# Performance work log

Measured on AMD Instinct MI355X. Metric: run time of the kernel, lower is better.

Reference implementation:

```python
import jax, jax.numpy as jnp
import numpy as np

N_NODES = 50000
N_EDGES = 800000
N_FIELDS = 4
N_MESH = 8
HIDDEN = 128
IN_CH = N_FIELDS * 1 + N_MESH  # 12


def _w(key, shape, scale=0.05):
    return jax.random.normal(key, shape, dtype=jnp.float32) * scale


def setup_inputs() -> dict:
    key = jax.random.key(0)
    ks = jax.random.split(key, 20)
    inp = {
        "F_0": jax.random.normal(ks[0], (N_NODES, 1, N_FIELDS), dtype=jnp.float32),
        "meshfield": jax.random.normal(ks[1], (N_NODES, N_MESH), dtype=jnp.float32),
        "edge_index": jax.random.randint(ks[2], (2, N_EDGES), 0, N_NODES, dtype=jnp.int32),
        "n_timesteps": 8,
        # encoder SAGEConv 1: in 12 -> 128 ; SAGEConv 2: 128 -> 128
        "enc1_Wl": _w(ks[3], (HIDDEN, IN_CH)), "enc1_bl": jnp.zeros((HIDDEN,), jnp.float32), "enc1_Wr": _w(ks[4], (HIDDEN, IN_CH)),
        "enc2_Wl": _w(ks[5], (HIDDEN, HIDDEN)), "enc2_bl": jnp.zeros((HIDDEN,), jnp.float32), "enc2_Wr": _w(ks[6], (HIDDEN, HIDDEN)),
        # decoder SAGEConv 1 & 2: 128 -> 128
        "dec1_Wl": _w(ks[7], (HIDDEN, HIDDEN)), "dec1_bl": jnp.zeros((HIDDEN,), jnp.float32), "dec1_Wr": _w(ks[8], (HIDDEN, HIDDEN)),
        "dec2_Wl": _w(ks[9], (HIDDEN, HIDDEN)), "dec2_bl": jnp.zeros((HIDDEN,), jnp.float32), "dec2_Wr": _w(ks[10], (HIDDEN, HIDDEN)),
        # output head: 128 -> n_fields
        "lin_W": _w(ks[11], (N_FIELDS, HIDDEN)), "lin_b": jnp.zeros((N_FIELDS,), jnp.float32),
    }
    return inp


def sage_conv(x, src, dst, Wl, bl, Wr, n_nodes):
    # PyG SAGEConv: out = lin_l(mean_j x_j) + lin_r(x_i); lin_l has bias, lin_r does not.
    msg = x[src]                                             # [E, C] gather
    agg = jax.ops.segment_sum(msg, dst, num_segments=n_nodes)
    cnt = jax.ops.segment_sum(jnp.ones((src.shape[0], 1), x.dtype), dst, num_segments=n_nodes)
    agg = agg / jnp.maximum(cnt, 1.0)                        # scatter-mean
    return agg @ Wl.T + bl + x @ Wr.T


def reference(F_0, meshfield, edge_index, n_timesteps,
              enc1_Wl, enc1_bl, enc1_Wr, enc2_Wl, enc2_bl, enc2_Wr,
              dec1_Wl, dec1_bl, dec1_Wr, dec2_Wl, dec2_bl, dec2_Wr,
              lin_W, lin_b):
    n = F_0.shape[0]
    src, dst = edge_index[0], edge_index[1]
    relu = jax.nn.relu
    F_prev = F_0  # [N, n_prev=1, n_fields]
    outs = []
    for _ in range(int(n_timesteps)):
        x_prev = F_prev[:, -1]                               # [N, n_fields]
        x = jnp.concatenate([F_prev.reshape(n, -1), meshfield], axis=1)  # [N, 12]
        # encoder GraphSAGE (act between layers, none after last)
        h = relu(sage_conv(x, src, dst, enc1_Wl, enc1_bl, enc1_Wr, n))
        h = sage_conv(h, src, dst, enc2_Wl, enc2_bl, enc2_Wr, n)
        h = relu(h)                                          # self.act after encoder
        # decoder GraphSAGE
        h = relu(sage_conv(h, src, dst, dec1_Wl, dec1_bl, dec1_Wr, n))
        h = sage_conv(h, src, dst, dec2_Wl, dec2_bl, dec2_Wr, n)
        h = relu(h)                                          # self.act after decoder
        x_new = x_prev + h @ lin_W.T + lin_b                 # residual update
        outs.append(x_new[:, None, :])
        # recurrence uses detached prediction (x.detach() in torch)
        F_prev = jnp.concatenate([F_prev[:, 1:], jax.lax.stop_gradient(x_new)[:, None, :]], axis=1)
    return jnp.concatenate(outs, axis=1)                     # [N, n_timesteps, n_fields]
```

## Files before the change

kernel.cpp:

```cpp
#include <hip/hip_runtime.h>


typedef __attribute__((ext_vector_type(8))) short short8;
typedef __attribute__((ext_vector_type(8))) unsigned short ushort8;
typedef __attribute__((ext_vector_type(4))) float f32x4;

static __device__ __forceinline__ float b2f(unsigned short u) {
  return __uint_as_float(((unsigned int)u) << 16);
}
static __device__ __forceinline__ unsigned short f2bf(float f) {
  unsigned int u = __float_as_uint(f);
  u += 0x7FFFu + ((u >> 16) & 1u);
  return (unsigned short)(u >> 16);
}


__global__ void count_rank_kernel(const int* __restrict__ dst, int* __restrict__ cnt,
                                  int* __restrict__ rank, int E) {
  int e = blockIdx.x * blockDim.x + threadIdx.x;
  if (e < E) rank[e] = atomicAdd(&cnt[dst[e]], 1);
}

__global__ __launch_bounds__(256) void blocksum_kernel(const int* __restrict__ cnt,
                                                       int* __restrict__ bsum, int n) {
  __shared__ int s[256];
  int tid = threadIdx.x;
  int i = blockIdx.x * 256 + tid;
  s[tid] = (i < n) ? cnt[i] : 0;
  __syncthreads();
  for (int off = 128; off > 0; off >>= 1) {
    if (tid < off) s[tid] += s[tid + off];
    __syncthreads();
  }
  if (tid == 0) bsum[blockIdx.x] = s[0];
}

__global__ __launch_bounds__(256) void scan_sums_kernel(const int* __restrict__ bsum,
                                                        int* __restrict__ boff, int nb) {
  __shared__ int s[256];
  int tid = threadIdx.x;
  int v = (tid < nb) ? bsum[tid] : 0;
  s[tid] = v;
  __syncthreads();
  for (int off = 1; off < 256; off <<= 1) {
    int t = (tid >= off) ? s[tid - off] : 0;
    __syncthreads();
    s[tid] += t;
    __syncthreads();
  }
  if (tid < nb) boff[tid] = s[tid] - v;
}

__global__ __launch_bounds__(256) void expand_kernel(const int* __restrict__ cnt,
                                                     const int* __restrict__ boff,
                                                     int* __restrict__ row_ptr,
                                                     float* __restrict__ rdeg, int n) {
  __shared__ int s[256];
  int tid = threadIdx.x;
  int i = blockIdx.x * 256 + tid;
  int v = (i < n) ? cnt[i] : 0;
  s[tid] = v;
  __syncthreads();
  for (int off = 1; off < 256; off <<= 1) {
    int t = (tid >= off) ? s[tid - off] : 0;
    __syncthreads();
    s[tid] += t;
    __syncthreads();
  }
  if (i < n) {
    row_ptr[i + 1] = boff[blockIdx.x] + s[tid];
    rdeg[i] = 1.0f / fmaxf((float)v, 1.0f);
  }
  if (i == 0) row_ptr[0] = 0;
}

__global__ void fill_csr2_kernel(const int* __restrict__ src, const int* __restrict__ dst,
                                 const int* __restrict__ rank, const int* __restrict__ row_ptr,
                                 int* __restrict__ col, int E) {
  int e = blockIdx.x * blockDim.x + threadIdx.x;
  if (e < E) col[row_ptr[dst[e]] + rank[e]] = src[e];
}

__global__ void f2bf6_kernel(const float* __restrict__ s0, const float* __restrict__ s1,
                             const float* __restrict__ s2, const float* __restrict__ s3,
                             const float* __restrict__ s4, const float* __restrict__ s5,
                             unsigned short* __restrict__ dst) {
  int i = blockIdx.x * blockDim.x + threadIdx.x;
  if (i >= 6 * 16384) return;
  int m = i >> 14, o = i & 16383;
  const float* s;
  switch (m) {
    case 0: s = s0; break; case 1: s = s1; break; case 2: s = s2; break;
    case 3: s = s3; break; case 4: s = s4; break; default: s = s5; break;
  }
  dst[i] = f2bf(s[o]);
}

__global__ void aggmesh_kernel(const float* __restrict__ mesh, float* __restrict__ aggm,
                               const int* __restrict__ row_ptr, const int* __restrict__ col,
                               const float* __restrict__ rdeg, int N) {
  int g = blockIdx.x * blockDim.x + threadIdx.x;
  int node = g >> 1, h = (g & 1) * 4;
  if (node >= N) return;
  int j0 = row_ptr[node], j1 = row_ptr[node + 1];
  float4 acc = make_float4(0.f, 0.f, 0.f, 0.f);
  int j = j0;
  for (; j + 4 <= j1; j += 4) {
    float4 v0 = *(const float4*)&mesh[col[j] * 8 + h];
    float4 v1 = *(const float4*)&mesh[col[j + 1] * 8 + h];
    float4 v2 = *(const float4*)&mesh[col[j + 2] * 8 + h];
    float4 v3 = *(const float4*)&mesh[col[j + 3] * 8 + h];
    acc.x += (v0.x + v1.x) + (v2.x + v3.x);
    acc.y += (v0.y + v1.y) + (v2.y + v3.y);
    acc.z += (v0.z + v1.z) + (v2.z + v3.z);
    acc.w += (v0.w + v1.w) + (v2.w + v3.w);
  }
  for (; j < j1; ++j) {
    float4 v0 = *(const float4*)&mesh[col[j] * 8 + h];
    acc.x += v0.x; acc.y += v0.y; acc.z += v0.z; acc.w += v0.w;
  }
  float r = rdeg[node];
  acc.x *= r; acc.y *= r; acc.z *= r; acc.w *= r;
  *(float4*)&aggm[node * 8 + h] = acc;
}

__global__ void mesh_term_kernel(const float* __restrict__ aggm, const float* __restrict__ mesh,
                                 const float* __restrict__ Wl, const float* __restrict__ Wr,
                                 const float* __restrict__ bl, unsigned short* __restrict__ mterm,
                                 int N) {
  int g = blockIdx.x * blockDim.x + threadIdx.x;
  if (g >= N * 128) return;
  int n = g >> 7, o = g & 127;
  float acc = bl[o];
#pragma unroll
  for (int k = 0; k < 8; ++k)
    acc += Wl[o * 12 + 4 + k] * aggm[n * 8 + k] + Wr[o * 12 + 4 + k] * mesh[n * 8 + k];
  mterm[g] = f2bf(acc);
}


__global__ __launch_bounds__(256) void enc1_kernel(
    const float* __restrict__ xprev, const int* __restrict__ row_ptr,
    const int* __restrict__ col, const float* __restrict__ rdeg,
    const float* __restrict__ Wl, const float* __restrict__ Wr,
    const unsigned short* __restrict__ mterm, unsigned short* __restrict__ out, int N) {
  __shared__ float Wx[8][128];
  __shared__ float4 part[256];
  __shared__ float As[64][8];
  int tid = threadIdx.x;
  int nb = blockIdx.x * 64;
  for (int i = tid; i < 1024; i += 256) {
    int k = i >> 7, o = i & 127;
    Wx[k][o] = (k < 4) ? Wl[o * 12 + k] : Wr[o * 12 + (k - 4)];
  }
  int nl = tid >> 2, q = tid & 3;
  int gn = nb + nl; if (gn > N - 1) gn = N - 1;
  int j0 = row_ptr[gn], j1 = row_ptr[gn + 1];
  int per = (j1 - j0 + 3) >> 2;
  int a = j0 + q * per; if (a > j1) a = j1;
  int b = a + per; if (b > j1) b = j1;
  float4 acc = make_float4(0.f, 0.f, 0.f, 0.f);
  int j = a;
  for (; j + 2 <= b; j += 2) {
    float4 v0 = *(const float4*)&xprev[col[j] * 4];
    float4 v1 = *(const float4*)&xprev[col[j + 1] * 4];
    acc.x += v0.x + v1.x; acc.y += v0.y + v1.y;
    acc.z += v0.z + v1.z; acc.w += v0.w + v1.w;
  }
  if (j < b) {
    float4 v0 = *(const float4*)&xprev[col[j] * 4];
    acc.x += v0.x; acc.y += v0.y; acc.z += v0.z; acc.w += v0.w;
  }
  part[tid] = acc;
  __syncthreads();
  if (tid < 64) {
    int g2 = nb + tid; if (g2 > N - 1) g2 = N - 1;
    float4 s0 = part[tid * 4], s1 = part[tid * 4 + 1];
    float4 s2 = part[tid * 4 + 2], s3 = part[tid * 4 + 3];
    float r = rdeg[g2];
    As[tid][0] = (s0.x + s1.x + s2.x + s3.x) * r;
    As[tid][1] = (s0.y + s1.y + s2.y + s3.y) * r;
    As[tid][2] = (s0.z + s1.z + s2.z + s3.z) * r;
    As[tid][3] = (s0.w + s1.w + s2.w + s3.w) * r;
    float4 own = *(const float4*)&xprev[g2 * 4];
    As[tid][4] = own.x; As[tid][5] = own.y; As[tid][6] = own.z; As[tid][7] = own.w;
  }
  __syncthreads();
  int gn2 = nb + nl;
  if (gn2 >= N) return;
  float av[8];
#pragma unroll
  for (int k = 0; k < 8; ++k) av[k] = As[nl][k];
  int o0 = q * 32;
#pragma unroll
  for (int c = 0; c < 4; ++c) {
    ushort8 mt = *(const ushort8*)&mterm[gn2 * 128 + o0 + c * 8];
    ushort8 ov;
#pragma unroll
    for (int oo = 0; oo < 8; ++oo) {
      int o = o0 + c * 8 + oo;
      float s = b2f(mt[oo]);
#pragma unroll
      for (int k = 0; k < 8; ++k) s += av[k] * Wx[k][o];
      ov[oo] = f2bf(fmaxf(s, 0.0f));
    }
    *(ushort8*)&out[gn2 * 128 + o0 + c * 8] = ov;
  }
}

__global__ void agg128_kernel(const unsigned short* __restrict__ feat,
                              unsigned short* __restrict__ out,
                              const int* __restrict__ row_ptr, const int* __restrict__ col,
                              const float* __restrict__ rdeg, int N) {
  int g = blockIdx.x * blockDim.x + threadIdx.x;
  int node = g >> 4;
  int d = g & 15;
  if (node >= N) return;
  int j0 = row_ptr[node], j1 = row_ptr[node + 1];
  float acc[8] = {};
  int j = j0;
  for (; j + 8 <= j1; j += 8) {
    ushort8 v0 = *(const ushort8*)&feat[col[j    ] * 128 + d * 8];
    ushort8 v1 = *(const ushort8*)&feat[col[j + 1] * 128 + d * 8];
    ushort8 v2 = *(const ushort8*)&feat[col[j + 2] * 128 + d * 8];
    ushort8 v3 = *(const ushort8*)&feat[col[j + 3] * 128 + d * 8];
    ushort8 v4 = *(const ushort8*)&feat[col[j + 4] * 128 + d * 8];
    ushort8 v5 = *(const ushort8*)&feat[col[j + 5] * 128 + d * 8];
    ushort8 v6 = *(const ushort8*)&feat[col[j + 6] * 128 + d * 8];
    ushort8 v7 = *(const ushort8*)&feat[col[j + 7] * 128 + d * 8];
#pragma unroll
    for (int r = 0; r < 8; ++r)
      acc[r] += ((b2f(v0[r]) + b2f(v1[r])) + (b2f(v2[r]) + b2f(v3[r]))) +
                ((b2f(v4[r]) + b2f(v5[r])) + (b2f(v6[r]) + b2f(v7[r])));
  }
  for (; j + 2 <= j1; j += 2) {
    ushort8 v0 = *(const ushort8*)&feat[col[j] * 128 + d * 8];
    ushort8 v1 = *(const ushort8*)&feat[col[j + 1] * 128 + d * 8];
#pragma unroll
    for (int r = 0; r < 8; ++r) acc[r] += b2f(v0[r]) + b2f(v1[r]);
  }
  if (j < j1) {
    ushort8 v0 = *(const ushort8*)&feat[col[j] * 128 + d * 8];
#pragma unroll
    for (int r = 0; r < 8; ++r) acc[r] += b2f(v0[r]);
  }
  float rd = rdeg[node];
  ushort8 o;
#pragma unroll
  for (int r = 0; r < 8; ++r) o[r] = f2bf(acc[r] * rd);
  *(ushort8*)&out[node * 128 + d * 8] = o;
}

__global__ __launch_bounds__(256) void gemm128_mfma_kernel(
    const unsigned short* __restrict__ agg, const unsigned short* __restrict__ x,
    const unsigned short* __restrict__ Wlb, const unsigned short* __restrict__ Wrb,
    const float* __restrict__ bl, unsigned short* __restrict__ out, int N) {
  int tid = threadIdx.x;
  int wave = tid >> 6;
  int lane = tid & 63;
  int nb = blockIdx.x * 128 + wave * 32;
  int l15 = lane & 15;
  int lk = (lane >> 4) * 8;

  f32x4 acc[2][8] = {};
  int r0 = nb + l15;      if (r0 > N - 1) r0 = N - 1;
  int r1 = nb + 16 + l15; if (r1 > N - 1) r1 = N - 1;

#pragma unroll
  for (int ks = 0; ks < 8; ++ks) {
    const unsigned short* As = (ks < 4) ? agg : x;
    const unsigned short* Ws = (ks < 4) ? Wlb : Wrb;
    int ko = (ks & 3) * 32 + lk;
    short8 a0 = *(const short8*)&As[r0 * 128 + ko];
    short8 a1 = *(const short8*)&As[r1 * 128 + ko];
#pragma unroll
    for (int ot = 0; ot < 8; ++ot) {
      short8 b = *(const short8*)&Ws[(ot * 16 + l15) * 128 + ko];
      acc[0][ot] = __builtin_amdgcn_mfma_f32_16x16x32_bf16(a0, b, acc[0][ot], 0, 0, 0);
      acc[1][ot] = __builtin_amdgcn_mfma_f32_16x16x32_bf16(a1, b, acc[1][ot], 0, 0, 0);
    }
  }

  int crow = (lane >> 4) * 4;
#pragma unroll
  for (int ot = 0; ot < 8; ++ot) {
    int gcol = ot * 16 + l15;
    float bv = bl[gcol];
#pragma unroll
    for (int mt = 0; mt < 2; ++mt) {
#pragma unroll
      for (int r = 0; r < 4; ++r) {
        int grow = nb + mt * 16 + crow + r;
        if (grow < N) {
          float v = fmaxf(acc[mt][ot][r] + bv, 0.0f);
          out[grow * 128 + gcol] = f2bf(v);
        }
      }
    }
  }
}

__global__ __launch_bounds__(256) void gemm128_head_mfma_kernel(
    const unsigned short* __restrict__ agg, const unsigned short* __restrict__ x,
    const unsigned short* __restrict__ Wlb, const unsigned short* __restrict__ Wrb,
    const float* __restrict__ bl, const float* __restrict__ linW,
    const float* __restrict__ linb, float* __restrict__ xprev,
    float* __restrict__ out, int N, int T, int t) {
  __shared__ float Wh[4][128];
  int tid = threadIdx.x;
  for (int i = tid; i < 512; i += 256) Wh[i >> 7][i & 127] = linW[i];
  __syncthreads();

  int wave = tid >> 6;
  int lane = tid & 63;
  int nb = blockIdx.x * 128 + wave * 32;
  int l15 = lane & 15;
  int lk = (lane >> 4) * 8;

  f32x4 acc[2][8] = {};
  int r0 = nb + l15;      if (r0 > N - 1) r0 = N - 1;
  int r1 = nb + 16 + l15; if (r1 > N - 1) r1 = N - 1;

#pragma unroll
  for (int ks = 0; ks < 8; ++ks) {
    const unsigned short* As = (ks < 4) ? agg : x;
    const unsigned short* Ws = (ks < 4) ? Wlb : Wrb;
    int ko = (ks & 3) * 32 + lk;
    short8 a0 = *(const short8*)&As[r0 * 128 + ko];
    short8 a1 = *(const short8*)&As[r1 * 128 + ko];
#pragma unroll
    for (int ot = 0; ot < 8; ++ot) {
      short8 b = *(const short8*)&Ws[(ot * 16 + l15) * 128 + ko];
      acc[0][ot] = __builtin_amdgcn_mfma_f32_16x16x32_bf16(a0, b, acc[0][ot], 0, 0, 0);
      acc[1][ot] = __builtin_amdgcn_mfma_f32_16x16x32_bf16(a1, b, acc[1][ot], 0, 0, 0);
    }
  }

  float part[2][4][4] = {};
#pragma unroll
  for (int ot = 0; ot < 8; ++ot) {
    int gcol = ot * 16 + l15;
    float bv = bl[gcol];
    float w0 = Wh[0][gcol], w1 = Wh[1][gcol], w2 = Wh[2][gcol], w3 = Wh[3][gcol];
#pragma unroll
    for (int mt = 0; mt < 2; ++mt)
#pragma unroll
      for (int r = 0; r < 4; ++r) {
        float hv = fmaxf(acc[mt][ot][r] + bv, 0.0f);
        part[mt][r][0] += hv * w0;
        part[mt][r][1] += hv * w1;
        part[mt][r][2] += hv * w2;
        part[mt][r][3] += hv * w3;
      }
  }
#pragma unroll
  for (int m = 1; m < 16; m <<= 1)
#pragma unroll
    for (int mt = 0; mt < 2; ++mt)
#pragma unroll
      for (int r = 0; r < 4; ++r)
#pragma unroll
        for (int o = 0; o < 4; ++o)
          part[mt][r][o] += __shfl_xor(part[mt][r][o], m, 64);

  if (l15 == 0) {
    int crow = (lane >> 4) * 4;
    float4 lb = *(const float4*)linb;
#pragma unroll
    for (int mt = 0; mt < 2; ++mt)
#pragma unroll
      for (int r = 0; r < 4; ++r) {
        int grow = nb + mt * 16 + crow + r;
        if (grow < N) {
          float4 xp = *(const float4*)&xprev[grow * 4];
          float4 xn;
          xn.x = xp.x + part[mt][r][0] + lb.x;
          xn.y = xp.y + part[mt][r][1] + lb.y;
          xn.z = xp.z + part[mt][r][2] + lb.z;
          xn.w = xp.w + part[mt][r][3] + lb.w;
          *(float4*)&out[(grow * T + t) * 4] = xn;
          *(float4*)&xprev[grow * 4] = xn;
        }
      }
  }
}

extern "C" void kernel_launch(void* const* d_in, const int* in_sizes, int n_in,
                              void* d_out, int out_size, void* d_ws, size_t ws_size,
                              hipStream_t stream) {
  const float* F0   = (const float*)d_in[0];
  const float* mesh = (const float*)d_in[1];
  const int*   eidx = (const int*)d_in[2];
  const float* e1Wl = (const float*)d_in[4];
  const float* e1bl = (const float*)d_in[5];
  const float* e1Wr = (const float*)d_in[6];
  const float* e2Wl = (const float*)d_in[7];
  const float* e2bl = (const float*)d_in[8];
  const float* e2Wr = (const float*)d_in[9];
  const float* d1Wl = (const float*)d_in[10];
  const float* d1bl = (const float*)d_in[11];
  const float* d1Wr = (const float*)d_in[12];
  const float* d2Wl = (const float*)d_in[13];
  const float* d2bl = (const float*)d_in[14];
  const float* d2Wr = (const float*)d_in[15];
  const float* linW = (const float*)d_in[16];
  const float* linb = (const float*)d_in[17];

  const int N = in_sizes[0] / 4;
  const int E = in_sizes[2] / 2;
  const int T = out_size / (N * 4);
  const int* src = eidx;
  const int* dst = eidx + E;

  size_t off = 0;
  auto alloc = [&](size_t bytes) -> void* {
    void* p = (char*)d_ws + off;
    off += (bytes + 511) & ~(size_t)511;
    return p;
  };
  int*   cnt     = (int*)alloc((size_t)N * 4);
  int*   row_ptr = (int*)alloc((size_t)(N + 1) * 4);
  int*   rank    = (int*)alloc((size_t)E * 4);
  int*   col     = (int*)alloc((size_t)E * 4);
  float* rdeg    = (float*)alloc((size_t)N * 4);
  float* xprev   = (float*)alloc((size_t)N * 4 * 4);
  float* aggm    = (float*)alloc((size_t)N * 8 * 4);
  int*   bsum    = (int*)alloc(256 * 4);
  int*   boff    = (int*)alloc(256 * 4);
  unsigned short* mterm = (unsigned short*)alloc((size_t)N * 128 * 2);
  unsigned short* h1   = (unsigned short*)alloc((size_t)N * 128 * 2);
  unsigned short* h2   = (unsigned short*)alloc((size_t)N * 128 * 2);
  unsigned short* aggb = (unsigned short*)alloc((size_t)N * 128 * 2);
  unsigned short* wb   = (unsigned short*)alloc((size_t)6 * 128 * 128 * 2);
  unsigned short* e2Wlb = wb + 0 * 16384;
  unsigned short* e2Wrb = wb + 1 * 16384;
  unsigned short* d1Wlb = wb + 2 * 16384;
  unsigned short* d1Wrb = wb + 3 * 16384;
  unsigned short* d2Wlb = wb + 4 * 16384;
  unsigned short* d2Wrb = wb + 5 * 16384;

  float* outp = (float*)d_out;

  const int NB = (N + 255) / 256;

  hipMemsetAsync(cnt, 0, (size_t)N * 4, stream);
  count_rank_kernel<<<(E + 255) / 256, 256, 0, stream>>>(dst, cnt, rank, E);
  blocksum_kernel<<<NB, 256, 0, stream>>>(cnt, bsum, N);
  scan_sums_kernel<<<1, 256, 0, stream>>>(bsum, boff, NB);
  expand_kernel<<<NB, 256, 0, stream>>>(cnt, boff, row_ptr, rdeg, N);
  fill_csr2_kernel<<<(E + 255) / 256, 256, 0, stream>>>(src, dst, rank, row_ptr, col, E);
  f2bf6_kernel<<<(6 * 16384 + 255) / 256, 256, 0, stream>>>(
      e2Wl, e2Wr, d1Wl, d1Wr, d2Wl, d2Wr, wb);
  aggmesh_kernel<<<(N * 2 + 255) / 256, 256, 0, stream>>>(mesh, aggm, row_ptr, col, rdeg, N);
  mesh_term_kernel<<<(N * 128 + 255) / 256, 256, 0, stream>>>(aggm, mesh, e1Wl, e1Wr, e1bl,
                                                              mterm, N);
  hipMemcpyAsync(xprev, F0, (size_t)N * 4 * 4, hipMemcpyDeviceToDevice, stream);

  const int gAgg  = (N * 16 + 255) / 256;
  const int gGemm = (N + 127) / 128;
  const int gEnc1 = (N + 63) / 64;

  for (int t = 0; t < T; ++t) {
    enc1_kernel<<<gEnc1, 256, 0, stream>>>(xprev, row_ptr, col, rdeg,
                                           e1Wl, e1Wr, mterm, h1, N);

    agg128_kernel<<<gAgg, 256, 0, stream>>>(h1, aggb, row_ptr, col, rdeg, N);
    gemm128_mfma_kernel<<<gGemm, 256, 0, stream>>>(aggb, h1, e2Wlb, e2Wrb, e2bl, h2, N);

    agg128_kernel<<<gAgg, 256, 0, stream>>>(h2, aggb, row_ptr, col, rdeg, N);
    gemm128_mfma_kernel<<<gGemm, 256, 0, stream>>>(aggb, h2, d1Wlb, d1Wrb, d1bl, h1, N);

    agg128_kernel<<<gAgg, 256, 0, stream>>>(h1, aggb, row_ptr, col, rdeg, N);
    gemm128_head_mfma_kernel<<<gGemm, 256, 0, stream>>>(aggb, h1, d2Wlb, d2Wrb, d2bl,
                                                        linW, linb, xprev, outp, N, T, t);
  }
}
```

Measured before the change: 1.642 ms.

## Fuse neighbor mean aggregation into MFMA GEMM via LDS staging

Merges the separate 128-channel gather-mean kernel and the MFMA GEMM kernel into one kernel per SAGE layer. Each block aggregates 64 nodes into padded LDS and then runs the bf16 MFMA GEMM straight from LDS, so the aggregated intermediate no longer makes a round trip through global memory and the kernel launch count drops. The trade-off is smaller GEMM tiles (16 rows per wave instead of 32), which reloads the weights more often, and the gather and GEMM phases now share a block's occupancy, which could reduce latency hiding during the irregular gathers.

```diff
diff --git a/kernel.cpp b/kernel.cpp
--- a/kernel.cpp
+++ b/kernel.cpp
@@ -208,16 +208,11 @@
   }
 }
 
-__global__ void agg128_kernel(const unsigned short* __restrict__ feat,
-                              unsigned short* __restrict__ out,
-                              const int* __restrict__ row_ptr, const int* __restrict__ col,
-                              const float* __restrict__ rdeg, int N) {
-  int g = blockIdx.x * blockDim.x + threadIdx.x;
-  int node = g >> 4;
-  int d = g & 15;
-  if (node >= N) return;
-  int j0 = row_ptr[node], j1 = row_ptr[node + 1];
-  float acc[8] = {};
+static __device__ __forceinline__ void gather_mean8(
+    const unsigned short* __restrict__ feat, const int* __restrict__ row_ptr,
+    const int* __restrict__ col, const float* __restrict__ rdeg,
+    int gn, int d, float* acc) {
+  int j0 = row_ptr[gn], j1 = row_ptr[gn + 1];
   int j = j0;
   for (; j + 8 <= j1; j += 8) {
     ushort8 v0 = *(const ushort8*)&feat[col[j    ] * 128 + d * 8];
@@ -244,144 +239,160 @@
 #pragma unroll
     for (int r = 0; r < 8; ++r) acc[r] += b2f(v0[r]);
   }
-  float rd = rdeg[node];
-  ushort8 o;
-#pragma unroll
-  for (int r = 0; r < 8; ++r) o[r] = f2bf(acc[r] * rd);
-  *(ushort8*)&out[node * 128 + d * 8] = o;
-}
-
-__global__ __launch_bounds__(256) void gemm128_mfma_kernel(
-    const unsigned short* __restrict__ agg, const unsigned short* __restrict__ x,
+  float rd = rdeg[gn];
+#pragma unroll
+  for (int r = 0; r < 8; ++r) acc[r] *= rd;
+}
+
+#define LDSTRIDE 136
+
+__global__ __launch_bounds__(256, 4) void conv_fused_kernel(
+    const unsigned short* __restrict__ h,
     const unsigned short* __restrict__ Wlb, const unsigned short* __restrict__ Wrb,
-    const float* __restrict__ bl, unsigned short* __restrict__ out, int N) {
-  int tid = threadIdx.x;
+    const float* __restrict__ bl,
+    const int* __restrict__ row_ptr, const int* __restrict__ col,
+    const float* __restrict__ rdeg,
+    unsigned short* __restrict__ out, int N) {
+  __shared__ unsigned short Alds[64 * LDSTRIDE];
+  int tid = threadIdx.x;
+  int nb = blockIdx.x * 64;
+  int d = tid & 15;
+#pragma unroll
+  for (int pass = 0; pass < 4; ++pass) {
+    int n = pass * 16 + (tid >> 4);
+    int gn = nb + n; if (gn > N - 1) gn = N - 1;
+    float acc[8] = {};
+    gather_mean8(h, row_ptr, col, rdeg, gn, d, acc);
+    ushort8 o;
+#pragma unroll
+    for (int r = 0; r < 8; ++r) o[r] = f2bf(acc[r]);
+    *(ushort8*)&Alds[n * LDSTRIDE + d * 8] = o;
+  }
+  __syncthreads();
   int wave = tid >> 6;
   int lane = tid & 63;
-  int nb = blockIdx.x * 128 + wave * 32;
+  int wbase = wave * 16;
   int l15 = lane & 15;
   int lk = (lane >> 4) * 8;
-
-  f32x4 acc[2][8] = {};
-  int r0 = nb + l15;      if (r0 > N - 1) r0 = N - 1;
-  int r1 = nb + 16 + l15; if (r1 > N - 1) r1 = N - 1;
-
+  int r0 = nb + wbase + l15; if (r0 > N - 1) r0 = N - 1;
+
+  f32x4 acc[8] = {};
 #pragma unroll
   for (int ks = 0; ks < 8; ++ks) {
-    const unsigned short* As = (ks < 4) ? agg : x;
+    short8 a;
+    if (ks < 4) a = *(const short8*)&Alds[(wbase + l15) * LDSTRIDE + ks * 32 + lk];
+    else        a = *(const short8*)&h[r0 * 128 + (ks - 4) * 32 + lk];
     const unsigned short* Ws = (ks < 4) ? Wlb : Wrb;
     int ko = (ks & 3) * 32 + lk;
-    short8 a0 = *(const short8*)&As[r0 * 128 + ko];
-    short8 a1 = *(const short8*)&As[r1 * 128 + ko];
 #pragma unroll
     for (int ot = 0; ot < 8; ++ot) {
       short8 b = *(const short8*)&Ws[(ot * 16 + l15) * 128 + ko];
-      acc[0][ot] = __builtin_amdgcn_mfma_f32_16x16x32_bf16(a0, b, acc[0][ot], 0, 0, 0);
-      acc[1][ot] = __builtin_amdgcn_mfma_f32_16x16x32_bf16(a1, b, acc[1][ot], 0, 0, 0);
-    }
-  }
-
+      acc[ot] = __builtin_amdgcn_mfma_f32_16x16x32_bf16(a, b, acc[ot], 0, 0, 0);
+    }
+  }
   int crow = (lane >> 4) * 4;
 #pragma unroll
   for (int ot = 0; ot < 8; ++ot) {
     int gcol = ot * 16 + l15;
     float bv = bl[gcol];
 #pragma unroll
-    for (int mt = 0; mt < 2; ++mt) {
-#pragma unroll
-      for (int r = 0; r < 4; ++r) {
-        int grow = nb + mt * 16 + crow + r;
-        if (grow < N) {
-          float v = fmaxf(acc[mt][ot][r] + bv, 0.0f);
-          out[grow * 128 + gcol] = f2bf(v);
-        }
+    for (int r = 0; r < 4; ++r) {
+      int grow = nb + wbase + crow + r;
+      if (grow < N) {
+        float v = fmaxf(acc[ot][r] + bv, 0.0f);
+        out[grow * 128 + gcol] = f2bf(v);
       }
     }
   }
 }
 
-__global__ __launch_bounds__(256) void gemm128_head_mfma_kernel(
-    const unsigned short* __restrict__ agg, const unsigned short* __restrict__ x,
+__global__ __launch_bounds__(256, 4) void conv_head_fused_kernel(
+    const unsigned short* __restrict__ h,
     const unsigned short* __restrict__ Wlb, const unsigned short* __restrict__ Wrb,
-    const float* __restrict__ bl, const float* __restrict__ linW,
-    const float* __restrict__ linb, float* __restrict__ xprev,
-    float* __restrict__ out, int N, int T, int t) {
+    const float* __restrict__ bl,
+    const int* __restrict__ row_ptr, const int* __restrict__ col,
+    const float* __restrict__ rdeg,
+    const float* __restrict__ linW, const float* __restrict__ linb,
+    float* __restrict__ xprev, float* __restrict__ out, int N, int T, int t) {
+  __shared__ unsigned short Alds[64 * LDSTRIDE];
   __shared__ float Wh[4][128];
   int tid = threadIdx.x;
   for (int i = tid; i < 512; i += 256) Wh[i >> 7][i & 127] = linW[i];
-  __syncthreads();
-
+  int nb = blockIdx.x * 64;
+  int d = tid & 15;
+#pragma unroll
+  for (int pass = 0; pass < 4; ++pass) {
+    int n = pass * 16 + (tid >> 4);
+    int gn = nb + n; if (gn > N - 1) gn = N - 1;
+    float acc[8] = {};
+    gather_mean8(h, row_ptr, col, rdeg, gn, d, acc);
+    ushort8 o;
+#pragma unroll
+    for (int r = 0; r < 8; ++r) o[r] = f2bf(acc[r]);
+    *(ushort8*)&Alds[n * LDSTRIDE + d * 8] = o;
+  }
+  __syncthreads();
   int wave = tid >> 6;
   int lane = tid & 63;
-  int nb = blockIdx.x * 128 + wave * 32;
+  int wbase = wave * 16;
   int l15 = lane & 15;
   int lk = (lane >> 4) * 8;
-
-  f32x4 acc[2][8] = {};
-  int r0 = nb + l15;      if (r0 > N - 1) r0 = N - 1;
-  int r1 = nb + 16 + l15; if (r1 > N - 1) r1 = N - 1;
-
+  int r0 = nb + wbase + l15; if (r0 > N - 1) r0 = N - 1;
+
+  f32x4 acc[8] = {};
 #pragma unroll
   for (int ks = 0; ks < 8; ++ks) {
-    const unsigned short* As = (ks < 4) ? agg : x;
+    short8 a;
+    if (ks < 4) a = *(const short8*)&Alds[(wbase + l15) * LDSTRIDE + ks * 32 + lk];
+    else        a = *(const short8*)&h[r0 * 128 + (ks - 4) * 32 + lk];
     const unsigned short* Ws = (ks < 4) ? Wlb : Wrb;
     int ko = (ks & 3) * 32 + lk;
-    short8 a0 = *(const short8*)&As[r0 * 128 + ko];
-    short8 a1 = *(const short8*)&As[r1 * 128 + ko];
 #pragma unroll
     for (int ot = 0; ot < 8; ++ot) {
       short8 b = *(const short8*)&Ws[(ot * 16 + l15) * 128 + ko];
-      acc[0][ot] = __builtin_amdgcn_mfma_f32_16x16x32_bf16(a0, b, acc[0][ot], 0, 0, 0);
-      acc[1][ot] = __builtin_amdgcn_mfma_f32_16x16x32_bf16(a1, b, acc[1][ot], 0, 0, 0);
-    }
-  }
-
-  float part[2][4][4] = {};
+      acc[ot] = __builtin_amdgcn_mfma_f32_16x16x32_bf16(a, b, acc[ot], 0, 0, 0);
+    }
+  }
+  float part[4][4] = {};
 #pragma unroll
   for (int ot = 0; ot < 8; ++ot) {
     int gcol = ot * 16 + l15;
     float bv = bl[gcol];
     float w0 = Wh[0][gcol], w1 = Wh[1][gcol], w2 = Wh[2][gcol], w3 = Wh[3][gcol];
 #pragma unroll
-    for (int mt = 0; mt < 2; ++mt)
-#pragma unroll
-      for (int r = 0; r < 4; ++r) {
-        float hv = fmaxf(acc[mt][ot][r] + bv, 0.0f);
-        part[mt][r][0] += hv * w0;
-        part[mt][r][1] += hv * w1;
-        part[mt][r][2] += hv * w2;
-        part[mt][r][3] += hv * w3;
-      }
+    for (int r = 0; r < 4; ++r) {
+      float hv = fmaxf(acc[ot][r] + bv, 0.0f);
+      part[r][0] += hv * w0;
+      part[r][1] += hv * w1;
+      part[r][2] += hv * w2;
+      part[r][3] += hv * w3;
+    }
   }
 #pragma unroll
   for (int m = 1; m < 16; m <<= 1)
 #pragma unroll
-    for (int mt = 0; mt < 2; ++mt)
-#pragma unroll
-      for (int r = 0; r < 4; ++r)
-#pragma unroll
-        for (int o = 0; o < 4; ++o)
-          part[mt][r][o] += __shfl_xor(part[mt][r][o], m, 64);
+    for (int r = 0; r < 4; ++r)
+#pragma unroll
+      for (int o = 0; o < 4; ++o)
+        part[r][o] += __shfl_xor(part[r][o], m, 64);
 
   if (l15 == 0) {
     int crow = (lane >> 4) * 4;
     float4 lb = *(const float4*)linb;
 #pragma unroll
-    for (int mt = 0; mt < 2; ++mt)
-#pragma unroll
-      for (int r = 0; r < 4; ++r) {
-        int grow = nb + mt * 16 + crow + r;
-        if (grow < N) {
-          float4 xp = *(const float4*)&xprev[grow * 4];
-          float4 xn;
-          xn.x = xp.x + part[mt][r][0] + lb.x;
-          xn.y = xp.y + part[mt][r][1] + lb.y;
-          xn.z = xp.z + part[mt][r][2] + lb.z;
-          xn.w = xp.w + part[mt][r][3] + lb.w;
-          *(float4*)&out[(grow * T + t) * 4] = xn;
-          *(float4*)&xprev[grow * 4] = xn;
-        }
+    for (int r = 0; r < 4; ++r) {
+      int grow = nb + wbase + crow + r;
+      if (grow < N) {
+        float4 xp = *(const float4*)&xprev[grow * 4];
+        float4 xn;
+        xn.x = xp.x + part[r][0] + lb.x;
+        xn.y = xp.y + part[r][1] + lb.y;
+        xn.z = xp.z + part[r][2] + lb.z;
+        xn.w = xp.w + part[r][3] + lb.w;
+        *(float4*)&out[(grow * T + t) * 4] = xn;
+        *(float4*)&xprev[grow * 4] = xn;
       }
+    }
   }
 }
 
@@ -430,7 +441,6 @@
   unsigned short* mterm = (unsigned short*)alloc((size_t)N * 128 * 2);
   unsigned short* h1   = (unsigned short*)alloc((size_t)N * 128 * 2);
   unsigned short* h2   = (unsigned short*)alloc((size_t)N * 128 * 2);
-  unsigned short* aggb = (unsigned short*)alloc((size_t)N * 128 * 2);
   unsigned short* wb   = (unsigned short*)alloc((size_t)6 * 128 * 128 * 2);
   unsigned short* e2Wlb = wb + 0 * 16384;
   unsigned short* e2Wrb = wb + 1 * 16384;
@@ -456,22 +466,18 @@
                                                               mterm, N);
   hipMemcpyAsync(xprev, F0, (size_t)N * 4 * 4, hipMemcpyDeviceToDevice, stream);
 
-  const int gAgg  = (N * 16 + 255) / 256;
-  const int gGemm = (N + 127) / 128;
+  const int gConv = (N + 63) / 64;
   const int gEnc1 = (N + 63) / 64;
 
   for (int t = 0; t < T; ++t) {
     enc1_kernel<<<gEnc1, 256, 0, stream>>>(xprev, row_ptr, col, rdeg,
                                            e1Wl, e1Wr, mterm, h1, N);
-
-    agg128_kernel<<<gAgg, 256, 0, stream>>>(h1, aggb, row_ptr, col, rdeg, N);
-    gemm128_mfma_kernel<<<gGemm, 256, 0, stream>>>(aggb, h1, e2Wlb, e2Wrb, e2bl, h2, N);
-
-    agg128_kernel<<<gAgg, 256, 0, stream>>>(h2, aggb, row_ptr, col, rdeg, N);
-    gemm128_mfma_kernel<<<gGemm, 256, 0, stream>>>(aggb, h2, d1Wlb, d1Wrb, d1bl, h1, N);
-
-    agg128_kernel<<<gAgg, 256, 0, stream>>>(h1, aggb, row_ptr, col, rdeg, N);
-    gemm128_head_mfma_kernel<<<gGemm, 256, 0, stream>>>(aggb, h1, d2Wlb, d2Wrb, d2bl,
-                                                        linW, linb, xprev, outp, N, T, t);
-  }
-}
+    conv_fused_kernel<<<gConv, 256, 0, stream>>>(h1, e2Wlb, e2Wrb, e2bl,
+                                                 row_ptr, col, rdeg, h2, N);
+    conv_fused_kernel<<<gConv, 256, 0, stream>>>(h2, d1Wlb, d1Wrb, d1bl,
+                                                 row_ptr, col, rdeg, h1, N);
+    conv_head_fused_kernel<<<gConv, 256, 0, stream>>>(h1, d2Wlb, d2Wrb, d2bl,
+                                                      row_ptr, col, rdeg,
+                                                      linW, linb, xprev, outp, N, T, t);
+  }
+}
```

Measured after the change: 1.705 ms. 1.04x slower.

## Slice hidden features into 4 column panels mapped to XCD pairs

Applied to the files above, without the earlier changes.

Stores the 128-wide bf16 hidden activations as four contiguous [N,32] column slices instead of row-major [N,128], and rewrites aggregation so that each pair of XCDs (chosen by block index modulo 8) handles a single slice. The goal is for each XCD's L2 to hold only a quarter of the feature table during the random neighbour gathers, which should raise the hit rate. Index and output accesses also gain nontemporal hints. The cost is narrower gathers per edge (4 threads per node in place of 16) and strided, scattered 2-byte stores in the GEMM epilogue, and the scheme depends on round-robin block-to-XCD placement.

```diff
diff --git a/kernel.cpp b/kernel.cpp
--- a/kernel.cpp
+++ b/kernel.cpp
@@ -147,6 +147,7 @@
   __shared__ float Wx[8][128];
   __shared__ float4 part[256];
   __shared__ float As[64][8];
+  size_t N32 = (size_t)N * 32;
   int tid = threadIdx.x;
   int nb = blockIdx.x * 64;
   for (int i = tid; i < 1024; i += 256) {
@@ -162,13 +163,15 @@
   float4 acc = make_float4(0.f, 0.f, 0.f, 0.f);
   int j = a;
   for (; j + 2 <= b; j += 2) {
-    float4 v0 = *(const float4*)&xprev[col[j] * 4];
-    float4 v1 = *(const float4*)&xprev[col[j + 1] * 4];
+    int s0 = __builtin_nontemporal_load(&col[j]);
+    int s1 = __builtin_nontemporal_load(&col[j + 1]);
+    float4 v0 = *(const float4*)&xprev[s0 * 4];
+    float4 v1 = *(const float4*)&xprev[s1 * 4];
     acc.x += v0.x + v1.x; acc.y += v0.y + v1.y;
     acc.z += v0.z + v1.z; acc.w += v0.w + v1.w;
   }
   if (j < b) {
-    float4 v0 = *(const float4*)&xprev[col[j] * 4];
+    float4 v0 = *(const float4*)&xprev[__builtin_nontemporal_load(&col[j]) * 4];
     acc.x += v0.x; acc.y += v0.y; acc.z += v0.z; acc.w += v0.w;
   }
   part[tid] = acc;
@@ -192,6 +195,7 @@
 #pragma unroll
   for (int k = 0; k < 8; ++k) av[k] = As[nl][k];
   int o0 = q * 32;
+  unsigned short* op = out + (size_t)q * N32 + (size_t)gn2 * 32;
 #pragma unroll
   for (int c = 0; c < 4; ++c) {
     ushort8 mt = *(const ushort8*)&mterm[gn2 * 128 + o0 + c * 8];
@@ -204,43 +208,42 @@
       for (int k = 0; k < 8; ++k) s += av[k] * Wx[k][o];
       ov[oo] = f2bf(fmaxf(s, 0.0f));
     }
-    *(ushort8*)&out[gn2 * 128 + o0 + c * 8] = ov;
-  }
-}
-
-__global__ void agg128_kernel(const unsigned short* __restrict__ feat,
-                              unsigned short* __restrict__ out,
-                              const int* __restrict__ row_ptr, const int* __restrict__ col,
-                              const float* __restrict__ rdeg, int N) {
-  int g = blockIdx.x * blockDim.x + threadIdx.x;
-  int node = g >> 4;
-  int d = g & 15;
+    __builtin_nontemporal_store(ov, (ushort8*)&op[c * 8]);
+  }
+}
+
+__global__ __launch_bounds__(256) void agg128_sliced_kernel(
+    const unsigned short* __restrict__ feat, unsigned short* __restrict__ out,
+    const int* __restrict__ row_ptr, const int* __restrict__ col,
+    const float* __restrict__ rdeg, int N) {
+  int b = blockIdx.x;
+  int xcd = b & 7;
+  int slice = xcd >> 1;
+  int chunk = (b >> 3) * 2 + (xcd & 1);
+  int node = chunk * 64 + (threadIdx.x >> 2);
   if (node >= N) return;
+  int d = threadIdx.x & 3;
+  size_t N32 = (size_t)N * 32;
+  const unsigned short* fp = feat + (size_t)slice * N32 + d * 8;
   int j0 = row_ptr[node], j1 = row_ptr[node + 1];
   float acc[8] = {};
   int j = j0;
-  for (; j + 8 <= j1; j += 8) {
-    ushort8 v0 = *(const ushort8*)&feat[col[j    ] * 128 + d * 8];
-    ushort8 v1 = *(const ushort8*)&feat[col[j + 1] * 128 + d * 8];
-    ushort8 v2 = *(const ushort8*)&feat[col[j + 2] * 128 + d * 8];
-    ushort8 v3 = *(const ushort8*)&feat[col[j + 3] * 128 + d * 8];
-    ushort8 v4 = *(const ushort8*)&feat[col[j + 4] * 128 + d * 8];
-    ushort8 v5 = *(const ushort8*)&feat[col[j + 5] * 128 + d * 8];
-    ushort8 v6 = *(const ushort8*)&feat[col[j + 6] * 128 + d * 8];
-    ushort8 v7 = *(const ushort8*)&feat[col[j + 7] * 128 + d * 8];
+  for (; j + 4 <= j1; j += 4) {
+    int s0 = __builtin_nontemporal_load(&col[j]);
+    int s1 = __builtin_nontemporal_load(&col[j + 1]);
+    int s2 = __builtin_nontemporal_load(&col[j + 2]);
+    int s3 = __builtin_nontemporal_load(&col[j + 3]);
+    ushort8 v0 = *(const ushort8*)&fp[(size_t)s0 * 32];
+    ushort8 v1 = *(const ushort8*)&fp[(size_t)s1 * 32];
+    ushort8 v2 = *(const ushort8*)&fp[(size_t)s2 * 32];
+    ushort8 v3 = *(const ushort8*)&fp[(size_t)s3 * 32];
 #pragma unroll
     for (int r = 0; r < 8; ++r)
-      acc[r] += ((b2f(v0[r]) + b2f(v1[r])) + (b2f(v2[r]) + b2f(v3[r]))) +
-                ((b2f(v4[r]) + b2f(v5[r])) + (b2f(v6[r]) + b2f(v7[r])));
-  }
-  for (; j + 2 <= j1; j += 2) {
-    ushort8 v0 = *(const ushort8*)&feat[col[j] * 128 + d * 8];
-    ushort8 v1 = *(const ushort8*)&feat[col[j + 1] * 128 + d * 8];
-#pragma unroll
-    for (int r = 0; r < 8; ++r) acc[r] += b2f(v0[r]) + b2f(v1[r]);
-  }
-  if (j < j1) {
-    ushort8 v0 = *(const ushort8*)&feat[col[j] * 128 + d * 8];
+      acc[r] += (b2f(v0[r]) + b2f(v1[r])) + (b2f(v2[r]) + b2f(v3[r]));
+  }
+  for (; j < j1; ++j) {
+    int s0 = __builtin_nontemporal_load(&col[j]);
+    ushort8 v0 = *(const ushort8*)&fp[(size_t)s0 * 32];
 #pragma unroll
     for (int r = 0; r < 8; ++r) acc[r] += b2f(v0[r]);
   }
@@ -248,13 +251,15 @@
   ushort8 o;
 #pragma unroll
   for (int r = 0; r < 8; ++r) o[r] = f2bf(acc[r] * rd);
-  *(ushort8*)&out[node * 128 + d * 8] = o;
+  __builtin_nontemporal_store(
+      o, (ushort8*)&out[(size_t)slice * N32 + (size_t)node * 32 + d * 8]);
 }
 
 __global__ __launch_bounds__(256) void gemm128_mfma_kernel(
     const unsigned short* __restrict__ agg, const unsigned short* __restrict__ x,
     const unsigned short* __restrict__ Wlb, const unsigned short* __restrict__ Wrb,
     const float* __restrict__ bl, unsigned short* __restrict__ out, int N) {
+  size_t N32 = (size_t)N * 32;
   int tid = threadIdx.x;
   int wave = tid >> 6;
   int lane = tid & 63;
@@ -268,11 +273,12 @@
 
 #pragma unroll
   for (int ks = 0; ks < 8; ++ks) {
-    const unsigned short* As = (ks < 4) ? agg : x;
+    const unsigned short* P = (ks < 4) ? (agg + (size_t)ks * N32)
+                                       : (x + (size_t)(ks - 4) * N32);
+    short8 a0 = *(const short8*)&P[(size_t)r0 * 32 + lk];
+    short8 a1 = *(const short8*)&P[(size_t)r1 * 32 + lk];
     const unsigned short* Ws = (ks < 4) ? Wlb : Wrb;
     int ko = (ks & 3) * 32 + lk;
-    short8 a0 = *(const short8*)&As[r0 * 128 + ko];
-    short8 a1 = *(const short8*)&As[r1 * 128 + ko];
 #pragma unroll
     for (int ot = 0; ot < 8; ++ot) {
       short8 b = *(const short8*)&Ws[(ot * 16 + l15) * 128 + ko];
@@ -286,6 +292,7 @@
   for (int ot = 0; ot < 8; ++ot) {
     int gcol = ot * 16 + l15;
     float bv = bl[gcol];
+    unsigned short* op = out + (size_t)(gcol >> 5) * N32 + (gcol & 31);
 #pragma unroll
     for (int mt = 0; mt < 2; ++mt) {
 #pragma unroll
@@ -293,7 +300,7 @@
         int grow = nb + mt * 16 + crow + r;
         if (grow < N) {
           float v = fmaxf(acc[mt][ot][r] + bv, 0.0f);
-          out[grow * 128 + gcol] = f2bf(v);
+          __builtin_nontemporal_store(f2bf(v), &op[(size_t)grow * 32]);
         }
       }
     }
@@ -307,6 +314,7 @@
     const float* __restrict__ linb, float* __restrict__ xprev,
     float* __restrict__ out, int N, int T, int t) {
   __shared__ float Wh[4][128];
+  size_t N32 = (size_t)N * 32;
   int tid = threadIdx.x;
   for (int i = tid; i < 512; i += 256) Wh[i >> 7][i & 127] = linW[i];
   __syncthreads();
@@ -323,11 +331,12 @@
 
 #pragma unroll
   for (int ks = 0; ks < 8; ++ks) {
-    const unsigned short* As = (ks < 4) ? agg : x;
+    const unsigned short* P = (ks < 4) ? (agg + (size_t)ks * N32)
+                                       : (x + (size_t)(ks - 4) * N32);
+    short8 a0 = *(const short8*)&P[(size_t)r0 * 32 + lk];
+    short8 a1 = *(const short8*)&P[(size_t)r1 * 32 + lk];
     const unsigned short* Ws = (ks < 4) ? Wlb : Wrb;
     int ko = (ks & 3) * 32 + lk;
-    short8 a0 = *(const short8*)&As[r0 * 128 + ko];
-    short8 a1 = *(const short8*)&As[r1 * 128 + ko];
 #pragma unroll
     for (int ot = 0; ot < 8; ++ot) {
       short8 b = *(const short8*)&Ws[(ot * 16 + l15) * 128 + ko];
@@ -456,7 +465,8 @@
                                                               mterm, N);
   hipMemcpyAsync(xprev, F0, (size_t)N * 4 * 4, hipMemcpyDeviceToDevice, stream);
 
-  const int gAgg  = (N * 16 + 255) / 256;
+  const int K = ((N + 63) / 64 + 1) / 2;
+  const int gAgg  = 8 * K;
   const int gGemm = (N + 127) / 128;
   const int gEnc1 = (N + 63) / 64;
 
@@ -464,13 +474,13 @@
     enc1_kernel<<<gEnc1, 256, 0, stream>>>(xprev, row_ptr, col, rdeg,
                                            e1Wl, e1Wr, mterm, h1, N);
 
-    agg128_kernel<<<gAgg, 256, 0, stream>>>(h1, aggb, row_ptr, col, rdeg, N);
+    agg128_sliced_kernel<<<gAgg, 256, 0, stream>>>(h1, aggb, row_ptr, col, rdeg, N);
     gemm128_mfma_kernel<<<gGemm, 256, 0, stream>>>(aggb, h1, e2Wlb, e2Wrb, e2bl, h2, N);
 
-    agg128_kernel<<<gAgg, 256, 0, stream>>>(h2, aggb, row_ptr, col, rdeg, N);
+    agg128_sliced_kernel<<<gAgg, 256, 0, stream>>>(h2, aggb, row_ptr, col, rdeg, N);
     gemm128_mfma_kernel<<<gGemm, 256, 0, stream>>>(aggb, h2, d1Wlb, d1Wrb, d1bl, h1, N);
 
-    agg128_kernel<<<gAgg, 256, 0, stream>>>(h1, aggb, row_ptr, col, rdeg, N);
+    agg128_sliced_kernel<<<gAgg, 256, 0, stream>>>(h1, aggb, row_ptr, col, rdeg, N);
     gemm128_head_mfma_kernel<<<gGemm, 256, 0, stream>>>(aggb, h1, d2Wlb, d2Wrb, d2bl,
                                                         linW, linb, xprev, outp, N, T, t);
   }
```

New measurement: 1.962 ms. 1.19x slower.

## Sort nodes by in-degree so aggregation wavefronts have balanced work

Applied to the files above, without the earlier changes.

Adds a one-time counting sort of nodes by in-degree (histogram, scan, scatter) and has agg128_kernel process nodes in that order through an indirection array. Nodes in the same wavefront then have similar edge counts, which cuts the divergence and idle lanes caused by mixed degrees. The cost is a few extra setup kernels, one extra indirect load per thread, and the loss of node-order locality for output writes and neighbour gathers.

```diff
diff --git a/kernel.cpp b/kernel.cpp
--- a/kernel.cpp
+++ b/kernel.cpp
@@ -79,6 +79,37 @@
                                  int* __restrict__ col, int E) {
   int e = blockIdx.x * blockDim.x + threadIdx.x;
   if (e < E) col[row_ptr[dst[e]] + rank[e]] = src[e];
+}
+
+__global__ void deg_hist_kernel(const int* __restrict__ cnt, int* __restrict__ hist, int N) {
+  int n = blockIdx.x * blockDim.x + threadIdx.x;
+  if (n < N) atomicAdd(&hist[min(cnt[n], 127)], 1);
+}
+
+__global__ __launch_bounds__(128) void scan128_kernel(const int* __restrict__ hist,
+                                                      int* __restrict__ binoff) {
+  __shared__ int s[128];
+  int tid = threadIdx.x;
+  int v = hist[tid];
+  s[tid] = v;
+  __syncthreads();
+  for (int off = 1; off < 128; off <<= 1) {
+    int t = (tid >= off) ? s[tid - off] : 0;
+    __syncthreads();
+    s[tid] += t;
+    __syncthreads();
+  }
+  binoff[tid] = s[tid] - v;
+}
+
+__global__ void scatter_order_kernel(const int* __restrict__ cnt, const int* __restrict__ binoff,
+                                     int* __restrict__ bincur, int* __restrict__ order, int N) {
+  int n = blockIdx.x * blockDim.x + threadIdx.x;
+  if (n < N) {
+    int d = min(cnt[n], 127);
+    int p = atomicAdd(&bincur[d], 1);
+    order[binoff[d] + p] = n;
+  }
 }
 
 __global__ void f2bf6_kernel(const float* __restrict__ s0, const float* __restrict__ s1,
@@ -211,11 +242,13 @@
 __global__ void agg128_kernel(const unsigned short* __restrict__ feat,
                               unsigned short* __restrict__ out,
                               const int* __restrict__ row_ptr, const int* __restrict__ col,
-                              const float* __restrict__ rdeg, int N) {
+                              const float* __restrict__ rdeg,
+                              const int* __restrict__ order, int N) {
   int g = blockIdx.x * blockDim.x + threadIdx.x;
-  int node = g >> 4;
+  int slot = g >> 4;
+  if (slot >= N) return;
+  int node = order[slot];
   int d = g & 15;
-  if (node >= N) return;
   int j0 = row_ptr[node], j1 = row_ptr[node + 1];
   float acc[8] = {};
   int j = j0;
@@ -427,6 +460,10 @@
   float* aggm    = (float*)alloc((size_t)N * 8 * 4);
   int*   bsum    = (int*)alloc(256 * 4);
   int*   boff    = (int*)alloc(256 * 4);
+  int*   hist    = (int*)alloc(128 * 4);
+  int*   binoff  = (int*)alloc(128 * 4);
+  int*   bincur  = (int*)alloc(128 * 4);
+  int*   order   = (int*)alloc((size_t)N * 4);
   unsigned short* mterm = (unsigned short*)alloc((size_t)N * 128 * 2);
   unsigned short* h1   = (unsigned short*)alloc((size_t)N * 128 * 2);
   unsigned short* h2   = (unsigned short*)alloc((size_t)N * 128 * 2);
@@ -444,11 +481,16 @@
   const int NB = (N + 255) / 256;
 
   hipMemsetAsync(cnt, 0, (size_t)N * 4, stream);
+  hipMemsetAsync(hist, 0, 128 * 4, stream);
+  hipMemsetAsync(bincur, 0, 128 * 4, stream);
   count_rank_kernel<<<(E + 255) / 256, 256, 0, stream>>>(dst, cnt, rank, E);
   blocksum_kernel<<<NB, 256, 0, stream>>>(cnt, bsum, N);
   scan_sums_kernel<<<1, 256, 0, stream>>>(bsum, boff, NB);
   expand_kernel<<<NB, 256, 0, stream>>>(cnt, boff, row_ptr, rdeg, N);
   fill_csr2_kernel<<<(E + 255) / 256, 256, 0, stream>>>(src, dst, rank, row_ptr, col, E);
+  deg_hist_kernel<<<NB, 256, 0, stream>>>(cnt, hist, N);
+  scan128_kernel<<<1, 128, 0, stream>>>(hist, binoff);
+  scatter_order_kernel<<<NB, 256, 0, stream>>>(cnt, binoff, bincur, order, N);
   f2bf6_kernel<<<(6 * 16384 + 255) / 256, 256, 0, stream>>>(
       e2Wl, e2Wr, d1Wl, d1Wr, d2Wl, d2Wr, wb);
   aggmesh_kernel<<<(N * 2 + 255) / 256, 256, 0, stream>>>(mesh, aggm, row_ptr, col, rdeg, N);
@@ -464,13 +506,13 @@
     enc1_kernel<<<gEnc1, 256, 0, stream>>>(xprev, row_ptr, col, rdeg,
                                            e1Wl, e1Wr, mterm, h1, N);
 
-    agg128_kernel<<<gAgg, 256, 0, stream>>>(h1, aggb, row_ptr, col, rdeg, N);
+    agg128_kernel<<<gAgg, 256, 0, stream>>>(h1, aggb, row_ptr, col, rdeg, order, N);
     gemm128_mfma_kernel<<<gGemm, 256, 0, stream>>>(aggb, h1, e2Wlb, e2Wrb, e2bl, h2, N);
 
-    agg128_kernel<<<gAgg, 256, 0, stream>>>(h2, aggb, row_ptr, col, rdeg, N);
+    agg128_kernel<<<gAgg, 256, 0, stream>>>(h2, aggb, row_ptr, col, rdeg, order, N);
     gemm128_mfma_kernel<<<gGemm, 256, 0, stream>>>(aggb, h2, d1Wlb, d1Wrb, d1bl, h1, N);
 
-    agg128_kernel<<<gAgg, 256, 0, stream>>>(h1, aggb, row_ptr, col, rdeg, N);
+    agg128_kernel<<<gAgg, 256, 0, stream>>>(h1, aggb, row_ptr, col, rdeg, order, N);
     gemm128_head_mfma_kernel<<<gGemm, 256, 0, stream>>>(aggb, h1, d2Wlb, d2Wrb, d2bl,
                                                         linW, linb, xprev, outp, N, T, t);
   }
```

After: 1.895 ms. +15.4%, slower.
